# Kernel optimization log

Measured on AMD Instinct MI355X. Metric: run time of the kernel, lower is better.

The kernel has to match this reference:

```python
import jax, jax.numpy as jnp
import numpy as np

S, B, L = 64, 32, 64          # seq_len (messages), batch (convs), max tokens per message
V, D = 32000, 300             # vocab, embedding dim
H = 512                       # hidden_dim; per-direction message hidden = H//2
F = 16                        # num_game_features
Hh = H // 2


def lstm_dir(x, mask, Wih, Whh, b, reverse=False):
    """Masked (packed-equivalent) LSTM. x:(T,N,D), mask:(T,N) bool.
    Returns h:(T,N,H) with zeros at invalid steps (matches pad_packed_sequence)."""
    if reverse:
        x, mask = x[::-1], mask[::-1]
    N = x.shape[1]
    Hd = Whh.shape[1]
    xg = jnp.einsum('tnd,gd->tng', x, Wih) + b  # (T,N,4H) input gates precomputed

    def step(carry, inp):
        h, c = carry
        xg_t, m = inp
        g = xg_t + h @ Whh.T
        i, f, gg, o = jnp.split(g, 4, axis=-1)
        c_new = jax.nn.sigmoid(f) * c + jax.nn.sigmoid(i) * jnp.tanh(gg)
        h_new = jax.nn.sigmoid(o) * jnp.tanh(c_new)
        m = m[:, None]
        return (jnp.where(m, h_new, h), jnp.where(m, c_new, c)), jnp.where(m, h_new, 0.0)

    init = (jnp.zeros((N, Hd), x.dtype), jnp.zeros((N, Hd), x.dtype))
    _, hs = jax.lax.scan(step, init, (xg, mask))
    if reverse:
        hs = hs[::-1]
    return hs


def setup_inputs() -> dict:
    key = jax.random.key(0)
    ks = jax.random.split(key, 16)
    s = 1.0 / np.sqrt(Hh)
    sc = 1.0 / np.sqrt(H)
    inp = {
        'messages': jax.random.randint(ks[0], (S, B, L), 0, V),
        'game_features': jax.random.normal(ks[1], (S, B, F), jnp.float32),
        'conv_lengths': jax.random.randint(ks[2], (B,), 1, S + 1),
        'E': jax.random.normal(ks[3], (V, D), jnp.float32) * 0.1,  # frozen embedding
        # message bi-LSTM (forward dir)
        'Wih_f': jax.random.uniform(ks[4], (4 * Hh, D), jnp.float32, -s, s),
        'Whh_f': jax.random.uniform(ks[5], (4 * Hh, Hh), jnp.float32, -s, s),
        'b_f': jax.random.uniform(ks[6], (4 * Hh,), jnp.float32, -s, s),
        # message bi-LSTM (backward dir)
        'Wih_b': jax.random.uniform(ks[7], (4 * Hh, D), jnp.float32, -s, s),
        'Whh_b': jax.random.uniform(ks[8], (4 * Hh, Hh), jnp.float32, -s, s),
        'b_b': jax.random.uniform(ks[9], (4 * Hh,), jnp.float32, -s, s),
        # conversation LSTM
        'Wih_c': jax.random.uniform(ks[10], (4 * H, H), jnp.float32, -sc, sc),
        'Whh_c': jax.random.uniform(ks[11], (4 * H, H), jnp.float32, -sc, sc),
        'b_c': jax.random.uniform(ks[12], (4 * H,), jnp.float32, -sc, sc),
        # classifier
        'Wc': jax.random.uniform(ks[13], (H + F,), jnp.float32, -sc, sc),
        'bc': jax.random.uniform(ks[14], (), jnp.float32, -sc, sc),
    }
    return inp


def reference(messages, game_features, conv_lengths, E, Wih_f, Whh_f, b_f,
              Wih_b, Whh_b, b_b, Wih_c, Whh_c, b_c, Wc, bc):
    # ---- message level: all S*B messages in one batched bi-LSTM pass ----
    flat = messages.reshape(S * B, L)                       # (N, L)
    emb = E[flat]                                           # (N, L, D)
    msg_len = jnp.maximum((flat != 0).sum(1), 1)            # clamp(min=1)
    tmask = jnp.arange(L)[:, None] < msg_len[None, :]       # (L, N)
    x = emb.transpose(1, 0, 2)                              # (L, N, D) time-major
    h_fwd = lstm_dir(x, tmask, Wih_f, Whh_f, b_f, reverse=False)
    h_bwd = lstm_dir(x, tmask, Wih_b, Whh_b, b_b, reverse=True)
    h = jnp.concatenate([h_fwd, h_bwd], axis=-1)            # (L, N, H); zeros at pad
    enc = h.max(axis=0)                                     # maxpool incl. zero pads (torch semantics)
    enc = enc.reshape(S, B, H)
    # ---- conversation level ----
    cmask = jnp.arange(S)[:, None] < conv_lengths[None, :]  # (S, B)
    conv_out = lstm_dir(enc, cmask, Wih_c, Whh_c, b_c)      # (S, B, H), zeros past length
    # dropout is identity at inference
    combined = jnp.concatenate([conv_out, game_features], axis=2)  # (S, B, H+F)
    logits = combined @ Wc + bc                             # (S, B)
    return logits
```

## Files before the change

kernel.cpp:

```cpp
#include <hip/hip_runtime.h>
#include <cmath>

#define S_DIM 64
#define B_DIM 32
#define L_DIM 64
#define NMSG  2048
#define D_DIM 300
#define HH    256
#define HC    512
#define F_DIM 16
#define VOCAB 32000

#define OFF_XGV   0u
#define OFF_WHH   32768000u
#define OFF_WPI   33030144u
#define OFF_WCI   33357824u
#define OFF_WCR   33882112u
#define OFF_ENCB  34406400u
#define OFF_HCONV 34930688u
#define OFF_CCONV 34938880u
#define OFF_CO    34955264u
#define OFF_MLEN  36003840u

typedef __attribute__((ext_vector_type(8))) short s8v;
typedef __attribute__((ext_vector_type(4))) float f4v;
#define MFMA(a,b,c) __builtin_amdgcn_mfma_f32_16x16x32_bf16((a),(b),(c),0,0,0)

__device__ __forceinline__ unsigned short f2bf(float x) {
    unsigned u = __float_as_uint(x);
    return (unsigned short)((u + 0x7FFFu + ((u >> 16) & 1u)) >> 16);
}
__device__ __forceinline__ float bf2f(unsigned short u) {
    return __uint_as_float(((unsigned)u) << 16);
}
__device__ __forceinline__ float sigm(float x) { return 1.0f / (1.0f + __expf(-x)); }
__device__ __forceinline__ float tanh_f(float x) { return 1.0f - 2.0f / (1.0f + __expf(2.0f * x)); }

__global__ __launch_bounds__(256) void pack_whh(
    const float* __restrict__ Whh_f, const float* __restrict__ Whh_b,
    unsigned short* __restrict__ Wp)
{
    int cg = blockIdx.x & 15, kt = blockIdx.x >> 4;
    int dir = blockIdx.y;
    const float* W = dir ? Whh_b : Whh_f;
    int tid = threadIdx.x, lane = tid & 63, g = tid >> 6;
    int wrow = g * 256 + cg * 16 + (lane & 15);
    int k0 = kt * 32 + (lane >> 4) * 8;
    unsigned short tmp[8];
    #pragma unroll
    for (int u = 0; u < 8; ++u) tmp[u] = f2bf(W[(size_t)wrow * HH + k0 + u]);
    *(uint4*)(Wp + ((((size_t)(dir * 16 + cg) * 8 + kt) * 4 + g) * 512) + lane * 8) = *(uint4*)tmp;
}

__global__ __launch_bounds__(256) void pack_wih(
    const float* __restrict__ Wih_f, const float* __restrict__ Wih_b,
    unsigned short* __restrict__ wpi)
{
    int nt = blockIdx.x, dir = blockIdx.y;
    const float* W = dir ? Wih_b : Wih_f;
    int tid = threadIdx.x, lane = tid & 63, ktq = tid >> 6;
    int n = nt * 16 + (lane & 15);
    int kb = (lane >> 4) * 8;
    for (int kt = ktq; kt < 10; kt += 4) {
        int k0 = kt * 32 + kb;
        unsigned short tmp[8];
        #pragma unroll
        for (int u = 0; u < 8; ++u) {
            int k = k0 + u;
            tmp[u] = (k < D_DIM) ? f2bf(W[(size_t)n * D_DIM + k]) : (unsigned short)0;
        }
        *(uint4*)(wpi + (size_t)dir * 327680 + ((size_t)(nt * 10 + kt)) * 512 + lane * 8) = *(uint4*)tmp;
    }
}

__global__ __launch_bounds__(256) void pack_whc(
    const float* __restrict__ Wih_c, const float* __restrict__ Whh_c,
    unsigned short* __restrict__ whci, unsigned short* __restrict__ whcr)
{
    int nt = blockIdx.x, which = blockIdx.y;
    const float* W = which ? Whh_c : Wih_c;
    unsigned short* dst = which ? whcr : whci;
    int tid = threadIdx.x, lane = tid & 63;
    int row = nt * 16 + (lane & 15);
    int kb = (lane >> 4) * 8;
    for (int kt = tid >> 6; kt < 16; kt += 4) {
        int k0 = kt * 32 + kb;
        unsigned short tmp[8];
        #pragma unroll
        for (int u = 0; u < 8; ++u) tmp[u] = f2bf(W[(size_t)row * HC + k0 + u]);
        *(uint4*)(dst + ((size_t)(nt * 16 + kt)) * 512 + lane * 8) = *(uint4*)tmp;
    }
}

__global__ __launch_bounds__(256) void msg_len_kernel(const int* __restrict__ msgs,
                                                      int* __restrict__ mlen) {
    int n = blockIdx.x * 256 + threadIdx.x;
    if (n >= NMSG) return;
    int cnt = 0;
    #pragma unroll 8
    for (int l = 0; l < L_DIM; ++l) cnt += (msgs[n * L_DIM + l] != 0);
    mlen[n] = max(cnt, 1);
}

__global__ __launch_bounds__(256) void init_conv(float* __restrict__ ws) {
    unsigned i = blockIdx.x * 256u + threadIdx.x;
    if (i < 24576u) ws[OFF_HCONV + i] = 0.0f;
}

#define EROW 328
__global__ __launch_bounds__(256) void xg_gemm(
    const float* __restrict__ E,
    const float* __restrict__ b_f, const float* __restrict__ b_b,
    const unsigned short* __restrict__ wpi,
    unsigned short* __restrict__ xgv)
{
    __shared__ __align__(16) unsigned short e_lds[32 * EROW];
    const int w0 = blockIdx.x * 32;
    const int dirb = blockIdx.y >> 2;
    const int jt = blockIdx.y & 3;
    const float* bias = dirb ? b_b : b_f;

    const int tid = threadIdx.x, lane = tid & 63, wv = tid >> 6;
    const int l15 = lane & 15, kg = lane >> 4;

    for (int i = tid; i < 32 * 320; i += 256) {
        int r = i / 320, k = i - r * 320;
        float v = (k < D_DIM) ? E[(size_t)(w0 + r) * D_DIM + k] : 0.0f;
        e_lds[r * EROW + k] = f2bf(v);
    }
    __syncthreads();

    const unsigned short* wb = wpi + (size_t)dirb * 327680;
    const f4v zf = {0.0f, 0.0f, 0.0f, 0.0f};
    f4v acc[2][4];
    #pragma unroll
    for (int m = 0; m < 2; ++m)
        #pragma unroll
        for (int g = 0; g < 4; ++g) acc[m][g] = zf;

    for (int kt = 0; kt < 10; ++kt) {
        s8v a0 = *(const s8v*)&e_lds[l15 * EROW + kt * 32 + kg * 8];
        s8v a1 = *(const s8v*)&e_lds[(16 + l15) * EROW + kt * 32 + kg * 8];
        #pragma unroll
        for (int g = 0; g < 4; ++g) {
            int nt = g * 16 + jt * 4 + wv;
            s8v b = *(const s8v*)(wb + ((size_t)(nt * 10 + kt)) * 512 + lane * 8);
            acc[0][g] = MFMA(a0, b, acc[0][g]);
            acc[1][g] = MFMA(a1, b, acc[1][g]);
        }
    }

    const int j = jt * 64 + wv * 16 + l15;
    float bv[4];
    #pragma unroll
    for (int g = 0; g < 4; ++g) bv[g] = bias[g * 256 + j];
    const int colp = (jt * 2 + (wv >> 1)) * 128 + l15 * 8 + (wv & 1) * 4;
    #pragma unroll
    for (int m = 0; m < 2; ++m)
        #pragma unroll
        for (int r = 0; r < 4; ++r) {
            int w = w0 + m * 16 + kg * 4 + r;
            unsigned short t4[4];
            #pragma unroll
            for (int g = 0; g < 4; ++g) t4[g] = f2bf(acc[m][g][r] + bv[g]);
            *(uint2*)(xgv + ((size_t)dirb * VOCAB + w) * 1024 + colp) = *(uint2*)t4;
        }
}

#define HROW 264
__global__ __launch_bounds__(1024, 4) void word_lstm(
    const int* __restrict__ msgs, const int* __restrict__ mlen,
    const unsigned short* __restrict__ xgv,
    const unsigned short* __restrict__ whh,
    unsigned short* __restrict__ enc_bf)
{
    __shared__ __align__(16) unsigned short h_lds[2][16 * HROW];
    __shared__ int tok_s[16 * 64];
    __shared__ int len_s[16];

    const int mg = blockIdx.x >> 1, dir = blockIdx.x & 1;
    const int tid = threadIdx.x, lane = tid & 63, cg = tid >> 6;
    const int l15 = lane & 15, kg = lane >> 4;

    for (int i = tid; i < 16 * 64; i += 1024) tok_s[i] = msgs[mg * 1024 + i];
    if (tid < 16) len_s[tid] = mlen[mg * 16 + tid];
    for (int i = tid; i < 2 * 16 * HROW; i += 1024) ((unsigned short*)h_lds)[i] = 0;
    __syncthreads();

    const unsigned short* xv = xgv + (size_t)dir * VOCAB * 1024;
    const unsigned short* wb = whh + (size_t)(dir * 16 + cg) * 16384 + lane * 8;
    const int qoff = (cg >> 1) * 128 + l15 * 8 + (cg & 1) * 4;

    int lens[4];
    #pragma unroll
    for (int r = 0; r < 4; ++r) lens[r] = len_s[kg * 4 + r];

    int bmax = 1;
    #pragma unroll
    for (int i = 0; i < 16; ++i) bmax = max(bmax, len_s[i]);

    float c_st[4], rm[4];
    unsigned short hbf[4];
    #pragma unroll
    for (int r = 0; r < 4; ++r) { c_st[r] = 0.0f; rm[r] = -INFINITY; hbf[r] = 0; }

    auto gather = [&](int t, uint2* q) {
        #pragma unroll
        for (int r = 0; r < 4; ++r) {
            int tt = dir ? (lens[r] - 1 - t) : t;
            if (tt < 0) tt = 0;
            q[r] = *(const uint2*)(xv + (size_t)tok_s[(kg * 4 + r) * 64 + tt] * 1024 + qoff);
        }
    };

    auto step = [&](int t, uint2* qc, uint2* qn) {
        __syncthreads();
        const int hbuf = t & 1;

        f4v acc[4];
        #pragma unroll
        for (int g = 0; g < 4; ++g) {
            f4v v;
            #pragma unroll
            for (int r = 0; r < 4; ++r)
                v[r] = bf2f(((const unsigned short*)&qc[r])[g]);
            acc[g] = v;
        }

        if (t + 1 < bmax) gather(t + 1, qn);

        #pragma unroll
        for (int kt = 0; kt < 8; ++kt) {
            s8v a = *(const s8v*)&h_lds[hbuf][l15 * HROW + kt * 32 + kg * 8];
            const unsigned short* pw = wb + kt * 2048;
            acc[0] = MFMA(a, *(const s8v*)(pw),        acc[0]);
            acc[1] = MFMA(a, *(const s8v*)(pw + 512),  acc[1]);
            acc[2] = MFMA(a, *(const s8v*)(pw + 1024), acc[2]);
            acc[3] = MFMA(a, *(const s8v*)(pw + 1536), acc[3]);
        }

        #pragma unroll
        for (int r = 0; r < 4; ++r) {
            float gi = acc[0][r], gf = acc[1][r], gc = acc[2][r], go = acc[3][r];
            float cn = sigm(gf) * c_st[r] + sigm(gi) * tanh_f(gc);
            float hn = sigm(go) * tanh_f(cn);
            if (t < lens[r]) {
                c_st[r] = cn;
                rm[r] = fmaxf(rm[r], hn);
                hbf[r] = f2bf(hn);
            }
            h_lds[hbuf ^ 1][(kg * 4 + r) * HROW + cg * 16 + l15] = hbf[r];
        }
    };

    uint2 qA[4], qB[4];
    gather(0, qA);
    for (int t = 0; t < bmax; t += 2) {
        step(t, qA, qB);
        if (t + 1 >= bmax) break;
        step(t + 1, qB, qA);
    }

    #pragma unroll
    for (int r = 0; r < 4; ++r) {
        float v = rm[r];
        if (lens[r] < 64) v = fmaxf(v, 0.0f);
        enc_bf[(size_t)(mg * 16 + kg * 4 + r) * HC + dir * HH + cg * 16 + l15] = f2bf(v);
    }
}

#define CROW 520
__global__ __launch_bounds__(256) void xgc_gemm(
    const unsigned short* __restrict__ enc_bf,
    const unsigned short* __restrict__ whci,
    const float* __restrict__ b_c,
    unsigned short* __restrict__ xgc)
{
    __shared__ __align__(16) unsigned short e_lds[32 * CROW];
    const int m0 = blockIdx.x * 32;
    const int n0 = blockIdx.y * 256;
    const int tid = threadIdx.x, lane = tid & 63, wv = tid >> 6;
    const int l15 = lane & 15, kg = lane >> 4;

    for (int i = tid; i < 2048; i += 256) {
        int row = i >> 6, u4 = i & 63;
        ((uint4*)&e_lds[row * CROW])[u4] = ((const uint4*)(enc_bf + (size_t)(m0 + row) * HC))[u4];
    }
    __syncthreads();

    const f4v zf = {0.0f, 0.0f, 0.0f, 0.0f};
    f4v acc[2][4];
    #pragma unroll
    for (int m = 0; m < 2; ++m)
        #pragma unroll
        for (int q = 0; q < 4; ++q) acc[m][q] = zf;

    for (int kt = 0; kt < 16; ++kt) {
        s8v a0 = *(const s8v*)&e_lds[l15 * CROW + kt * 32 + kg * 8];
        s8v a1 = *(const s8v*)&e_lds[(16 + l15) * CROW + kt * 32 + kg * 8];
        #pragma unroll
        for (int q = 0; q < 4; ++q) {
            int nt = (n0 >> 4) + wv * 4 + q;
            s8v b = *(const s8v*)(whci + ((size_t)(nt * 16 + kt)) * 512 + lane * 8);
            acc[0][q] = MFMA(a0, b, acc[0][q]);
            acc[1][q] = MFMA(a1, b, acc[1][q]);
        }
    }

    #pragma unroll
    for (int q = 0; q < 4; ++q) {
        int col = n0 + (wv * 4 + q) * 16 + l15;
        float bv = b_c[col];
        #pragma unroll
        for (int m = 0; m < 2; ++m)
            #pragma unroll
            for (int r = 0; r < 4; ++r)
                xgc[(size_t)(m0 + m * 16 + kg * 4 + r) * 2048 + col] = f2bf(acc[m][q][r] + bv);
    }
}

__global__ __launch_bounds__(256) void conv_step(
    const unsigned short* __restrict__ whcr,
    const unsigned short* __restrict__ xgc,
    const int* __restrict__ conv_len,
    unsigned short* __restrict__ h_bf,
    float* __restrict__ c_ws,
    float* __restrict__ co,
    int s)
{
    __shared__ __align__(16) unsigned short xh[32 * CROW];
    __shared__ float gbuf[4][32][16];

    const int tid = threadIdx.x, jb = blockIdx.x;
    const int lane = tid & 63, g = tid >> 6;
    const int l15 = lane & 15, kg = lane >> 4;

    for (int i = tid; i < 2048; i += 256) {
        int row = i >> 6, u4 = i & 63;
        ((uint4*)&xh[row * CROW])[u4] = ((const uint4*)(h_bf + (size_t)row * HC))[u4];
    }
    __syncthreads();

    const int col = g * 512 + jb * 16 + l15;
    f4v acc0, acc1;
    #pragma unroll
    for (int r = 0; r < 4; ++r) {
        acc0[r] = bf2f(xgc[(size_t)(s * B_DIM + kg * 4 + r) * 2048 + col]);
        acc1[r] = bf2f(xgc[(size_t)(s * B_DIM + 16 + kg * 4 + r) * 2048 + col]);
    }

    const int nt = g * 32 + jb;
    for (int kt = 0; kt < 16; ++kt) {
        s8v a0 = *(const s8v*)&xh[l15 * CROW + kt * 32 + kg * 8];
        s8v a1 = *(const s8v*)&xh[(16 + l15) * CROW + kt * 32 + kg * 8];
        s8v b  = *(const s8v*)(whcr + ((size_t)(nt * 16 + kt)) * 512 + lane * 8);
        acc0 = MFMA(a0, b, acc0);
        acc1 = MFMA(a1, b, acc1);
    }

    #pragma unroll
    for (int r = 0; r < 4; ++r) {
        gbuf[g][kg * 4 + r][l15]      = acc0[r];
        gbuf[g][16 + kg * 4 + r][l15] = acc1[r];
    }
    __syncthreads();

    #pragma unroll
    for (int u = 0; u < 2; ++u) {
        int cell = tid + 256 * u;
        int b = cell >> 4, jj = cell & 15;
        int j = jb * 16 + jj;
        bool valid = s < conv_len[b];
        float g_i = gbuf[0][b][jj], g_f = gbuf[1][b][jj];
        float g_c = gbuf[2][b][jj], g_o = gbuf[3][b][jj];
        float cold = c_ws[b * HC + j];
        float cn = sigm(g_f) * cold + sigm(g_i) * tanh_f(g_c);
        float hn = sigm(g_o) * tanh_f(cn);
        float outv = 0.0f;
        if (valid) {
            c_ws[b * HC + j] = cn;
            h_bf[b * HC + j] = f2bf(hn);
            outv = hn;
        }
        co[((size_t)s * B_DIM + b) * HC + j] = outv;
    }
}

__global__ __launch_bounds__(256) void logits_kernel(
    const float* __restrict__ gfeat, const float* __restrict__ Wc, const float* __restrict__ bc,
    const float* __restrict__ co, float* __restrict__ out)
{
    int o = blockIdx.x * 4 + (threadIdx.x >> 6);
    int lane = threadIdx.x & 63;
    const float* row = co + (size_t)o * HC;
    float sum = 0.0f;
    #pragma unroll
    for (int u = 0; u < 8; ++u) sum += row[lane + 64 * u] * Wc[lane + 64 * u];
    if (lane < F_DIM) sum += gfeat[o * F_DIM + lane] * Wc[HC + lane];
    #pragma unroll
    for (int off = 32; off > 0; off >>= 1) sum += __shfl_down(sum, off, 64);
    if (lane == 0) out[o] = sum + bc[0];
}

extern "C" void kernel_launch(void* const* d_in, const int* in_sizes, int n_in,
                              void* d_out, int out_size, void* d_ws, size_t ws_size,
                              hipStream_t stream) {
    const int*   msgs    = (const int*)  d_in[0];
    const float* gfeat   = (const float*)d_in[1];
    const int*   convlen = (const int*)  d_in[2];
    const float* E       = (const float*)d_in[3];
    const float* Wih_f   = (const float*)d_in[4];
    const float* Whh_f   = (const float*)d_in[5];
    const float* b_f     = (const float*)d_in[6];
    const float* Wih_b   = (const float*)d_in[7];
    const float* Whh_b   = (const float*)d_in[8];
    const float* b_b     = (const float*)d_in[9];
    const float* Wih_c   = (const float*)d_in[10];
    const float* Whh_c   = (const float*)d_in[11];
    const float* b_c     = (const float*)d_in[12];
    const float* Wc      = (const float*)d_in[13];
    const float* bc      = (const float*)d_in[14];
    float* out = (float*)d_out;
    float* ws  = (float*)d_ws;

    unsigned short* xgv    = (unsigned short*)(ws + OFF_XGV);
    unsigned short* xgc    = (unsigned short*)(ws + OFF_XGV);
    unsigned short* whh    = (unsigned short*)(ws + OFF_WHH);
    unsigned short* wpi    = (unsigned short*)(ws + OFF_WPI);
    unsigned short* whci   = (unsigned short*)(ws + OFF_WCI);
    unsigned short* whcr   = (unsigned short*)(ws + OFF_WCR);
    unsigned short* enc_bf = (unsigned short*)(ws + OFF_ENCB);
    unsigned short* h_bf   = (unsigned short*)(ws + OFF_HCONV);
    float*          c_ws   = ws + OFF_CCONV;
    float*          co     = ws + OFF_CO;
    int*            mlen   = (int*)(ws + OFF_MLEN);

    pack_whh<<<dim3(128, 2), 256, 0, stream>>>(Whh_f, Whh_b, whh);
    pack_wih<<<dim3(64, 2), 256, 0, stream>>>(Wih_f, Wih_b, wpi);
    pack_whc<<<dim3(128, 2), 256, 0, stream>>>(Wih_c, Whh_c, whci, whcr);
    msg_len_kernel<<<NMSG / 256, 256, 0, stream>>>(msgs, mlen);
    init_conv<<<96, 256, 0, stream>>>(ws);
    xg_gemm<<<dim3(1000, 8), 256, 0, stream>>>(E, b_f, b_b, wpi, xgv);

    word_lstm<<<256, 1024, 0, stream>>>(msgs, mlen, xgv, whh, enc_bf);

    xgc_gemm<<<dim3(64, 8), 256, 0, stream>>>(enc_bf, whci, b_c, xgc);

    for (int s = 0; s < S_DIM; ++s)
        conv_step<<<32, 256, 0, stream>>>(whcr, xgc, convlen, h_bf, c_ws, co, s);

    logits_kernel<<<NMSG / 4, 256, 0, stream>>>(gfeat, Wc, bc, co, out);
}
```

Measured before the change: 1.267 ms.

## Stage word-LSTM input gates via async global-to-LDS loads; fuse xg_gemm column tiles

```diff
diff --git a/kernel.cpp b/kernel.cpp
--- a/kernel.cpp
+++ b/kernel.cpp
@@ -36,20 +36,25 @@
 __device__ __forceinline__ float sigm(float x) { return 1.0f / (1.0f + __expf(-x)); }
 __device__ __forceinline__ float tanh_f(float x) { return 1.0f - 2.0f / (1.0f + __expf(2.0f * x)); }
 
+__device__ __forceinline__ void gload16(const unsigned short* g, unsigned short* l) {
+    __builtin_amdgcn_global_load_lds(
+        (const __attribute__((address_space(1))) unsigned int*)g,
+        (__attribute__((address_space(3))) unsigned int*)l, 16, 0, 0);
+}
+
 __global__ __launch_bounds__(256) void pack_whh(
     const float* __restrict__ Whh_f, const float* __restrict__ Whh_b,
     unsigned short* __restrict__ Wp)
 {
-    int cg = blockIdx.x & 15, kt = blockIdx.x >> 4;
-    int dir = blockIdx.y;
+    int wv = blockIdx.x >> 3, kt = blockIdx.x & 7, dir = blockIdx.y;
     const float* W = dir ? Whh_b : Whh_f;
     int tid = threadIdx.x, lane = tid & 63, g = tid >> 6;
-    int wrow = g * 256 + cg * 16 + (lane & 15);
+    int n = (g * 16 + wv) * 16 + (lane & 15);
     int k0 = kt * 32 + (lane >> 4) * 8;
     unsigned short tmp[8];
     #pragma unroll
-    for (int u = 0; u < 8; ++u) tmp[u] = f2bf(W[(size_t)wrow * HH + k0 + u]);
-    *(uint4*)(Wp + ((((size_t)(dir * 16 + cg) * 8 + kt) * 4 + g) * 512) + lane * 8) = *(uint4*)tmp;
+    for (int u = 0; u < 8; ++u) tmp[u] = f2bf(W[(size_t)n * HH + k0 + u]);
+    *(uint4*)(Wp + (((size_t)(dir * 16 + wv) * 8 + kt) * 4 + g) * 512 + lane * 8) = *(uint4*)tmp;
 }
 
 __global__ __launch_bounds__(256) void pack_wih(
@@ -116,80 +121,102 @@
 {
     __shared__ __align__(16) unsigned short e_lds[32 * EROW];
     const int w0 = blockIdx.x * 32;
-    const int dirb = blockIdx.y >> 2;
-    const int jt = blockIdx.y & 3;
+    const int dirb = blockIdx.y;
     const float* bias = dirb ? b_b : b_f;
 
     const int tid = threadIdx.x, lane = tid & 63, wv = tid >> 6;
     const int l15 = lane & 15, kg = lane >> 4;
 
-    for (int i = tid; i < 32 * 320; i += 256) {
-        int r = i / 320, k = i - r * 320;
-        float v = (k < D_DIM) ? E[(size_t)(w0 + r) * D_DIM + k] : 0.0f;
-        e_lds[r * EROW + k] = f2bf(v);
+    {
+        const float4* E4 = (const float4*)(E + (size_t)w0 * D_DIM);
+        for (int i = tid; i < 32 * 75; i += 256) {
+            int r = i / 75, c = i - r * 75;
+            float4 v = E4[r * 75 + c];
+            unsigned short t4[4] = { f2bf(v.x), f2bf(v.y), f2bf(v.z), f2bf(v.w) };
+            *(uint2*)&e_lds[r * EROW + c * 4] = *(uint2*)t4;
+        }
+        for (int i = tid; i < 32 * 20; i += 256) {
+            int r = i / 20, c = i - r * 20;
+            e_lds[r * EROW + 300 + c] = 0;
+        }
     }
     __syncthreads();
+
+    s8v a0q[10], a1q[10];
+    #pragma unroll
+    for (int kt = 0; kt < 10; ++kt) {
+        a0q[kt] = *(const s8v*)&e_lds[l15 * EROW + kt * 32 + kg * 8];
+        a1q[kt] = *(const s8v*)&e_lds[(16 + l15) * EROW + kt * 32 + kg * 8];
+    }
 
     const unsigned short* wb = wpi + (size_t)dirb * 327680;
     const f4v zf = {0.0f, 0.0f, 0.0f, 0.0f};
-    f4v acc[2][4];
-    #pragma unroll
-    for (int m = 0; m < 2; ++m)
-        #pragma unroll
-        for (int g = 0; g < 4; ++g) acc[m][g] = zf;
-
-    for (int kt = 0; kt < 10; ++kt) {
-        s8v a0 = *(const s8v*)&e_lds[l15 * EROW + kt * 32 + kg * 8];
-        s8v a1 = *(const s8v*)&e_lds[(16 + l15) * EROW + kt * 32 + kg * 8];
-        #pragma unroll
-        for (int g = 0; g < 4; ++g) {
-            int nt = g * 16 + jt * 4 + wv;
-            s8v b = *(const s8v*)(wb + ((size_t)(nt * 10 + kt)) * 512 + lane * 8);
-            acc[0][g] = MFMA(a0, b, acc[0][g]);
-            acc[1][g] = MFMA(a1, b, acc[1][g]);
-        }
-    }
-
-    const int j = jt * 64 + wv * 16 + l15;
-    float bv[4];
-    #pragma unroll
-    for (int g = 0; g < 4; ++g) bv[g] = bias[g * 256 + j];
-    const int colp = (jt * 2 + (wv >> 1)) * 128 + l15 * 8 + (wv & 1) * 4;
-    #pragma unroll
-    for (int m = 0; m < 2; ++m)
-        #pragma unroll
-        for (int r = 0; r < 4; ++r) {
-            int w = w0 + m * 16 + kg * 4 + r;
-            unsigned short t4[4];
-            #pragma unroll
-            for (int g = 0; g < 4; ++g) t4[g] = f2bf(acc[m][g][r] + bv[g]);
-            *(uint2*)(xgv + ((size_t)dirb * VOCAB + w) * 1024 + colp) = *(uint2*)t4;
-        }
-}
-
+
+    #pragma unroll
+    for (int jt = 0; jt < 4; ++jt) {
+        f4v acc[2][4];
+        #pragma unroll
+        for (int m = 0; m < 2; ++m)
+            #pragma unroll
+            for (int g = 0; g < 4; ++g) acc[m][g] = zf;
+
+        #pragma unroll
+        for (int kt = 0; kt < 10; ++kt) {
+            #pragma unroll
+            for (int g = 0; g < 4; ++g) {
+                int nt = g * 16 + jt * 4 + wv;
+                s8v b = *(const s8v*)(wb + ((size_t)(nt * 10 + kt)) * 512 + lane * 8);
+                acc[0][g] = MFMA(a0q[kt], b, acc[0][g]);
+                acc[1][g] = MFMA(a1q[kt], b, acc[1][g]);
+            }
+        }
+
+        const int j = jt * 64 + wv * 16 + l15;
+        float bv[4];
+        #pragma unroll
+        for (int g = 0; g < 4; ++g) bv[g] = bias[g * 256 + j];
+        const int colp = (jt * 2 + (wv >> 1)) * 128 + l15 * 8 + (wv & 1) * 4;
+        #pragma unroll
+        for (int m = 0; m < 2; ++m)
+            #pragma unroll
+            for (int r = 0; r < 4; ++r) {
+                int w = w0 + m * 16 + kg * 4 + r;
+                unsigned short t4[4];
+                #pragma unroll
+                for (int g = 0; g < 4; ++g) t4[g] = f2bf(acc[m][g][r] + bv[g]);
+                *(uint2*)(xgv + ((size_t)dirb * VOCAB + w) * 1024 + colp) = *(uint2*)t4;
+            }
+    }
+}
+
+#define XGS  1032
 #define HROW 264
-__global__ __launch_bounds__(1024, 4) void word_lstm(
+__global__ __launch_bounds__(1024, 1) void word_lstm(
     const int* __restrict__ msgs, const int* __restrict__ mlen,
     const unsigned short* __restrict__ xgv,
     const unsigned short* __restrict__ whh,
     unsigned short* __restrict__ enc_bf)
 {
+    __shared__ __align__(16) unsigned short xg_lds[2][16 * XGS];
     __shared__ __align__(16) unsigned short h_lds[2][16 * HROW];
     __shared__ int tok_s[16 * 64];
     __shared__ int len_s[16];
 
     const int mg = blockIdx.x >> 1, dir = blockIdx.x & 1;
-    const int tid = threadIdx.x, lane = tid & 63, cg = tid >> 6;
+    const int tid = threadIdx.x, lane = tid & 63, wv = tid >> 6;
     const int l15 = lane & 15, kg = lane >> 4;
 
     for (int i = tid; i < 16 * 64; i += 1024) tok_s[i] = msgs[mg * 1024 + i];
     if (tid < 16) len_s[tid] = mlen[mg * 16 + tid];
-    for (int i = tid; i < 2 * 16 * HROW; i += 1024) ((unsigned short*)h_lds)[i] = 0;
+    for (int i = tid; i < 2 * 16 * HROW; i += 1024) h_lds[0][i] = 0;
     __syncthreads();
 
     const unsigned short* xv = xgv + (size_t)dir * VOCAB * 1024;
-    const unsigned short* wb = whh + (size_t)(dir * 16 + cg) * 16384 + lane * 8;
-    const int qoff = (cg >> 1) * 128 + l15 * 8 + (cg & 1) * 4;
+
+    const unsigned short* wbase = whh + (size_t)(dir * 16 + wv) * 16384 + lane * 8;
+    const unsigned short* bp[8];
+    #pragma unroll
+    for (int kt = 0; kt < 8; ++kt) bp[kt] = wbase + kt * 2048;
 
     int lens[4];
     #pragma unroll
@@ -204,35 +231,53 @@
     #pragma unroll
     for (int r = 0; r < 4; ++r) { c_st[r] = 0.0f; rm[r] = -INFINITY; hbf[r] = 0; }
 
-    auto gather = [&](int t, uint2* q) {
-        #pragma unroll
-        for (int r = 0; r < 4; ++r) {
-            int tt = dir ? (lens[r] - 1 - t) : t;
+    const int qoff = (wv >> 1) * 128 + l15 * 8 + (wv & 1) * 4;
+
+    {
+        int tt = dir ? (len_s[wv] - 1) : 0;
+        if (tt < 0) tt = 0;
+        const unsigned short* src = xv + (size_t)tok_s[wv * 64 + tt] * 1024 + lane * 8;
+        gload16(src,       &xg_lds[0][wv * XGS]);
+        gload16(src + 512, &xg_lds[0][wv * XGS + 512]);
+    }
+
+    for (int t = 0; t < bmax; ++t) {
+        __syncthreads();
+        const int buf = t & 1;
+        const int hbuf = t & 1;
+
+        if (t + 1 < bmax) {
+            int tn = t + 1;
+            int tt = dir ? (len_s[wv] - 1 - tn) : tn;
             if (tt < 0) tt = 0;
-            q[r] = *(const uint2*)(xv + (size_t)tok_s[(kg * 4 + r) * 64 + tt] * 1024 + qoff);
-        }
-    };
-
-    auto step = [&](int t, uint2* qc, uint2* qn) {
-        __syncthreads();
-        const int hbuf = t & 1;
+            const unsigned short* src = xv + (size_t)tok_s[wv * 64 + tt] * 1024 + lane * 8;
+            gload16(src,       &xg_lds[buf ^ 1][wv * XGS]);
+            gload16(src + 512, &xg_lds[buf ^ 1][wv * XGS + 512]);
+        }
 
         f4v acc[4];
-        #pragma unroll
-        for (int g = 0; g < 4; ++g) {
-            f4v v;
+        {
+            uint2 q[4];
             #pragma unroll
             for (int r = 0; r < 4; ++r)
-                v[r] = bf2f(((const unsigned short*)&qc[r])[g]);
-            acc[g] = v;
-        }
-
-        if (t + 1 < bmax) gather(t + 1, qn);
+                q[r] = *(const uint2*)&xg_lds[buf][(kg * 4 + r) * XGS + qoff];
+            #pragma unroll
+            for (int g = 0; g < 4; ++g) {
+                f4v v;
+                #pragma unroll
+                for (int r = 0; r < 4; ++r) {
+                    unsigned w = (g & 2) ? q[r].y : q[r].x;
+                    v[r] = (g & 1) ? __uint_as_float(w & 0xFFFF0000u)
+                                   : __uint_as_float(w << 16);
+                }
+                acc[g] = v;
+            }
+        }
 
         #pragma unroll
         for (int kt = 0; kt < 8; ++kt) {
             s8v a = *(const s8v*)&h_lds[hbuf][l15 * HROW + kt * 32 + kg * 8];
-            const unsigned short* pw = wb + kt * 2048;
+            const unsigned short* pw = bp[kt];
             acc[0] = MFMA(a, *(const s8v*)(pw),        acc[0]);
             acc[1] = MFMA(a, *(const s8v*)(pw + 512),  acc[1]);
             acc[2] = MFMA(a, *(const s8v*)(pw + 1024), acc[2]);
@@ -249,23 +294,15 @@
                 rm[r] = fmaxf(rm[r], hn);
                 hbf[r] = f2bf(hn);
             }
-            h_lds[hbuf ^ 1][(kg * 4 + r) * HROW + cg * 16 + l15] = hbf[r];
-        }
-    };
-
-    uint2 qA[4], qB[4];
-    gather(0, qA);
-    for (int t = 0; t < bmax; t += 2) {
-        step(t, qA, qB);
-        if (t + 1 >= bmax) break;
-        step(t + 1, qB, qA);
+            h_lds[hbuf ^ 1][(kg * 4 + r) * HROW + wv * 16 + l15] = hbf[r];
+        }
     }
 
     #pragma unroll
     for (int r = 0; r < 4; ++r) {
         float v = rm[r];
         if (lens[r] < 64) v = fmaxf(v, 0.0f);
-        enc_bf[(size_t)(mg * 16 + kg * 4 + r) * HC + dir * HH + cg * 16 + l15] = f2bf(v);
+        enc_bf[(size_t)(mg * 16 + kg * 4 + r) * HC + dir * HH + wv * 16 + l15] = f2bf(v);
     }
 }
 
@@ -440,7 +477,7 @@
     pack_whc<<<dim3(128, 2), 256, 0, stream>>>(Wih_c, Whh_c, whci, whcr);
     msg_len_kernel<<<NMSG / 256, 256, 0, stream>>>(msgs, mlen);
     init_conv<<<96, 256, 0, stream>>>(ws);
-    xg_gemm<<<dim3(1000, 8), 256, 0, stream>>>(E, b_f, b_b, wpi, xgv);
+    xg_gemm<<<dim3(1000, 2), 256, 0, stream>>>(E, b_f, b_b, wpi, xgv);
 
     word_lstm<<<256, 1024, 0, stream>>>(msgs, mlen, xgv, whh, enc_bf);
 
```

New measurement: 1.157 ms (median of 2 runs). 1.1x faster.
